# Kernel optimization log

Measured on AMD Instinct MI355X. Metric: run time of the kernel, lower is better.

## Reference

```python
import jax, jax.numpy as jnp
import numpy as np

MAXHD, MAXV, MINA, MAXA, DT = 100.0, 40.0, -4.0, 3.0, 0.1
NVEH, NT, H = 16384, 256, 20


def setup_inputs() -> dict:
    key = jax.random.key(0)
    ks = jax.random.split(key, 6)
    lead_speed = 10.0 + 5.0 * jax.random.normal(ks[0], (NVEH, NT), dtype=jnp.float32)
    lead_pos = 50.0 + 20.0 * jax.random.normal(ks[1], (NVEH, NT), dtype=jnp.float32)
    lead_inputs = jnp.stack([lead_pos, lead_speed], axis=2)  # (nveh, nt, 2)
    init_state = jnp.stack([
        5.0 * jax.random.normal(ks[2], (NVEH,), dtype=jnp.float32),
        10.0 + 2.0 * jax.random.normal(ks[3], (NVEH,), dtype=jnp.float32),
    ], axis=1)  # (nveh, 2) -> (pos, speed)
    return {
        "lead_inputs": lead_inputs,
        "init_state": init_state,
        "h0": jnp.zeros((NVEH, H), jnp.float32),
        "c0": jnp.zeros((NVEH, H), jnp.float32),
        "W": 0.3 * jax.random.normal(ks[4], (3, 4 * H), dtype=jnp.float32),
        "U": 0.2 * jax.random.normal(ks[5], (H, 4 * H), dtype=jnp.float32),
        "b": jnp.concatenate([jnp.zeros(H), jnp.ones(H), jnp.zeros(2 * H)]).astype(jnp.float32),  # unit forget bias
        "Wd": 0.3 * jax.random.normal(jax.random.fold_in(key, 7), (H, 1), dtype=jnp.float32),
        "bd": jnp.zeros((1,), jnp.float32),
    }


def reference(lead_inputs, init_state, h0, c0, W, U, b, Wd, bd):
    def step(carry, lead):
        pos, speed, h, c = carry
        curhd = (lead[:, 0] - pos) / MAXHD
        lead_v = lead[:, 1] / MAXV
        norm_v = speed / MAXV
        x = jnp.stack([curhd, norm_v, lead_v], axis=1)  # (nveh, 3)
        z = x @ W + h @ U + b  # (nveh, 4H), keras gate order i, f, g, o
        i, f, g, o = jnp.split(z, 4, axis=1)
        c = jax.nn.sigmoid(f) * c + jax.nn.sigmoid(i) * jnp.tanh(g)
        h = jax.nn.sigmoid(o) * jnp.tanh(c)
        out = (h @ Wd + bd)[:, 0]  # (nveh,)
        acc = (MAXA - MINA) * out + MINA
        speed = speed + DT * acc
        pos = pos + DT * acc  # faithful to source (uses acc, not speed)
        return (pos, speed, h, c), pos

    pos0, speed0 = init_state[:, 0], init_state[:, 1]
    (pos, speed, h, c), ys = jax.lax.scan(
        step, (pos0, speed0, h0, c0), jnp.swapaxes(lead_inputs, 0, 1))
    # tf.concat of nt (nveh,) tensors along -1 -> flat (nt*nveh,) in time-major order
    outputs = ys.reshape(-1)
    return outputs, speed, (h, c)
```

## Files before the change

### kernel.cpp

```cpp
#include <hip/hip_runtime.h>


#define NVEH 16384
#define NT   256
#define H    20

typedef float f32x4  __attribute__((ext_vector_type(4)));
typedef short bf16x8 __attribute__((ext_vector_type(8)));

#if __has_builtin(__builtin_amdgcn_exp2f)
#define EXP2(x) __builtin_amdgcn_exp2f(x)
#else
#define EXP2(x) __expf((x) * 0.69314718056f)
#endif
#define RCP(x) __builtin_amdgcn_rcpf(x)

__device__ __forceinline__ short f2bf(float f) {
    unsigned u = __builtin_bit_cast(unsigned, f);
    u += 0x7fffu + ((u >> 16) & 1u);
    return (short)(u >> 16);
}
__device__ __forceinline__ float bf2f(short s) {
    return __builtin_bit_cast(float, ((unsigned)(unsigned short)s) << 16);
}

__global__ __launch_bounds__(256, 1) void rnncf_kernel(
    const float* __restrict__ lead,
    const float* __restrict__ inits,
    const float* __restrict__ h0,
    const float* __restrict__ c0,
    const float* __restrict__ W,
    const float* __restrict__ U,
    const float* __restrict__ b,
    const float* __restrict__ Wd,
    const float* __restrict__ bd,
    float* __restrict__ out)
{
    __shared__ __attribute__((aligned(16))) short UT[96 * 32];

    const int tid  = threadIdx.x;
    const int lane = tid & 63;
    const int q    = lane >> 4;
    const int c    = lane & 15;
    const float L2E = 1.44269504f;
    const float N2L = -2.f * L2E;
    const float P2L =  2.f * L2E;
    const float IN2L = -0.34657359028f;
    const float bdv = bd[0];
    const float biasK = 7.f * bdv - 4.f;

    for (int idx = tid; idx < 96 * 32; idx += 256) {
        int row = idx >> 5, k = idx & 31;
        int T = row >> 4, m = row & 15;
        int kq = k >> 3, ko = k & 7;
        float v = 0.f;
        if (T < 5) {
            int g = m & 3, j = 5 * (m >> 2) + T;
            int col = g * 20 + j;
            if      (ko < 5)             v = U[(5 * kq + ko) * 80 + col];
            else if (ko == 6 && kq < 3)  v = W[kq * 80 + col];
            else if (ko == 6)            v = b[col];
            v *= (g == 2) ? (2.f * L2E) : L2E;
        } else if ((m & 3) == 0) {
            if      (ko < 5)  v = 7.f * Wd[5 * kq + ko];
            else if (ko == 5) v = 1.f;
        }
        UT[idx] = f2bf(v);
    }

    const int veh = blockIdx.x * 64 + (tid >> 6) * 16 + c;

    float wcn[5][4], wd7[5], w7b[5];
#pragma unroll
    for (int T = 0; T < 5; ++T) {
        int j = 5 * q + T;
#pragma unroll
        for (int g = 0; g < 4; ++g) {
            int col = g * 20 + j;
            wcn[T][g] = -(-0.001f * W[col] + 0.0025f * W[80 + col])
                      * ((g == 2) ? (2.f * L2E) : L2E);
        }
        float w7 = 7.f * Wd[j];
        wd7[T] = w7;
        w7b[T] = bf2f(f2bf(w7));
    }

    bf16x8 Bf = {0, 0, 0, 0, 0, 0, 0, 0};
    float cst2[5], hl[5];
    float rpart = 0.f, apart = 0.f;
#pragma unroll
    for (int T = 0; T < 5; ++T) {
        int j = 5 * q + T;
        float hv = h0[veh * H + j];
        cst2[T] = N2L * c0[veh * H + j];
        hl[T] = hv;
        short hb = f2bf(hv);
        float hi = bf2f(hb);
        Bf[T] = hb;
        rpart = __builtin_fmaf(hv, wd7[T], rpart);
        rpart = __builtin_fmaf(-hi, w7b[T], rpart);
        apart = __builtin_fmaf(hv, wd7[T], apart);
    }
    Bf[5] = f2bf(rpart);
    apart += __shfl_xor(apart, 16);
    apart += __shfl_xor(apart, 32);

    float pos = inits[veh * 2 + 0];
    float spd = inits[veh * 2 + 1];
    {
        float a = apart + biasK;
        pos -= 0.1f * a;
        spd -= 0.1f * a;
    }

    const float2* lp0 = (const float2*)lead + (long)veh * NT;
    {
        float2 lu = lp0[0];
        float xv = (q == 0) ? (lu.x - pos) * 0.01f
                 : (q == 1) ? spd * 0.025f
                            : lu.y * 0.025f;
        if (q < 3) Bf[6] = f2bf(xv);
        else       Bf[6] = (short)0x3F80;
    }
    float2 lA = lp0[1];
    float2 lB = lp0[2];

    __syncthreads();

    bf16x8 A[6];
#pragma unroll
    for (int T = 0; T < 6; ++T)
        A[T] = *(const bf16x8*)&UT[(T * 16 + c) * 32 + q * 8];

    for (int t = 0; t < NT; ++t) {
        float2 lu = lA;
        lA = lB;
        int tn = t + 3; tn = (tn < NT) ? tn : NT - 1;
        lB = lp0[tn];

        f32x4 zero = {0.f, 0.f, 0.f, 0.f};
        f32x4 z5 = __builtin_amdgcn_mfma_f32_16x16x32_bf16(A[5], Bf, zero, 0, 0, 0);
        f32x4 z[5];
#pragma unroll
        for (int T = 0; T < 5; ++T)
            z[T] = __builtin_amdgcn_mfma_f32_16x16x32_bf16(A[T], Bf, zero, 0, 0, 0);

        float acc = z5[0] + biasK;
        pos = __builtin_fmaf(0.1f, acc, pos);
        spd = __builtin_fmaf(0.1f, acc, spd);
        if (q == 1 && t > 0)
            out[(size_t)(t - 1) * NVEH + veh] = pos;

        {
            float xv = (q == 0) ? (lu.x - pos) * 0.01f
                     : (q == 1) ? spd * 0.025f
                                : lu.y * 0.025f;
            if (q < 3) Bf[6] = f2bf(xv);
        }

        float rq = 0.f;
#pragma unroll
        for (int T = 0; T < 5; ++T) {
            float ei = EXP2(__builtin_fmaf(acc, wcn[T][0], -z[T][0]));
            float ef = EXP2(__builtin_fmaf(acc, wcn[T][1], -z[T][1]));
            float eg = EXP2(__builtin_fmaf(acc, wcn[T][2], -z[T][2]));
            float eo = EXP2(__builtin_fmaf(acc, wcn[T][3], -z[T][3]));
            float ff  = RCP(1.f + ef);
            float Rig = RCP((1.f + ei) * (1.f + eg));
            float uu  = __builtin_fmaf(P2L, eg, N2L);
            float c2  = __builtin_fmaf(ff, cst2[T], uu * Rig);
            cst2[T] = c2;
            float ec = EXP2(__builtin_fminf(c2, 80.f));
            float Roc = RCP((1.f + eo) * (1.f + ec));
            float hh = (1.f - ec) * Roc;
            hl[T] = hh;
            unsigned u = __builtin_bit_cast(unsigned, hh);
            unsigned r = u + 0x7fffu + ((u >> 16) & 1u);
            Bf[T] = (short)(r >> 16);
            float hi = __builtin_bit_cast(float, r & 0xffff0000u);
            rq = __builtin_fmaf(hh, wd7[T], rq);
            rq = __builtin_fmaf(-hi, w7b[T], rq);
        }
        Bf[5] = f2bf(rq);
    }

    float ap = 0.f;
#pragma unroll
    for (int T = 0; T < 5; ++T) ap = __builtin_fmaf(hl[T], wd7[T], ap);
    ap += __shfl_xor(ap, 16);
    ap += __shfl_xor(ap, 32);
    float accF = ap + biasK;
    if (q == 1) out[(size_t)(NT - 1) * NVEH + veh] = pos + 0.1f * accF;
    if (q == 2) out[(size_t)NT * NVEH + veh]       = spd + 0.1f * accF;

    const int oH = NT * NVEH + NVEH;
    const int oC = oH + NVEH * H;
#pragma unroll
    for (int T = 0; T < 5; ++T) {
        int j = 5 * q + T;
        out[oH + veh * H + j] = hl[T];
        out[oC + veh * H + j] = cst2[T] * IN2L;
    }
}

extern "C" void kernel_launch(void* const* d_in, const int* in_sizes, int n_in,
                              void* d_out, int out_size, void* d_ws, size_t ws_size,
                              hipStream_t stream) {
    const float* lead  = (const float*)d_in[0];
    const float* inits = (const float*)d_in[1];
    const float* h0    = (const float*)d_in[2];
    const float* c0    = (const float*)d_in[3];
    const float* W     = (const float*)d_in[4];
    const float* U     = (const float*)d_in[5];
    const float* b     = (const float*)d_in[6];
    const float* Wd    = (const float*)d_in[7];
    const float* bd    = (const float*)d_in[8];
    float* out = (float*)d_out;

    rnncf_kernel<<<NVEH / 64, 256, 0, stream>>>(lead, inits, h0, c0, W, U, b, Wd, bd, out);
}
```

Measured before the change: 210.0 us.

## Replace MFMA-folded dense output with in-loop shuffle reduction and simpler gate math

Removes the sixth MFMA tile that folded the dense output projection and its bf16 residual correction into the recurrent matmul. The acceleration correction terms (wcn) that compensated for the one-step lag are dropped. Acceleration is now computed exactly each step with a per-lane dot product and two cross-lane shuffles. The gate update is also restructured to use a single combined reciprocal for the forget/input/cell gates. This puts the shuffle reduction back on the serial critical path of every step, in exchange for one fewer MFMA and fewer FMAs and reciprocals.

```diff
diff --git a/kernel.cpp b/kernel.cpp
--- a/kernel.cpp
+++ b/kernel.cpp
@@ -20,9 +20,6 @@
     u += 0x7fffu + ((u >> 16) & 1u);
     return (short)(u >> 16);
 }
-__device__ __forceinline__ float bf2f(short s) {
-    return __builtin_bit_cast(float, ((unsigned)(unsigned short)s) << 16);
-}
 
 __global__ __launch_bounds__(256, 1) void rnncf_kernel(
     const float* __restrict__ lead,
@@ -36,7 +33,7 @@
     const float* __restrict__ bd,
     float* __restrict__ out)
 {
-    __shared__ __attribute__((aligned(16))) short UT[96 * 32];
+    __shared__ __attribute__((aligned(16))) short UT[80 * 32];
 
     const int tid  = threadIdx.x;
     const int lane = tid & 63;
@@ -46,72 +43,41 @@
     const float N2L = -2.f * L2E;
     const float P2L =  2.f * L2E;
     const float IN2L = -0.34657359028f;
-    const float bdv = bd[0];
-    const float biasK = 7.f * bdv - 4.f;
+    const float biasK = 7.f * bd[0] - 4.f;
 
-    for (int idx = tid; idx < 96 * 32; idx += 256) {
+    for (int idx = tid; idx < 80 * 32; idx += 256) {
         int row = idx >> 5, k = idx & 31;
         int T = row >> 4, m = row & 15;
         int kq = k >> 3, ko = k & 7;
+        int g = m & 3, j = 5 * (m >> 2) + T;
+        int col = g * 20 + j;
         float v = 0.f;
-        if (T < 5) {
-            int g = m & 3, j = 5 * (m >> 2) + T;
-            int col = g * 20 + j;
-            if      (ko < 5)             v = U[(5 * kq + ko) * 80 + col];
-            else if (ko == 6 && kq < 3)  v = W[kq * 80 + col];
-            else if (ko == 6)            v = b[col];
-            v *= (g == 2) ? (2.f * L2E) : L2E;
-        } else if ((m & 3) == 0) {
-            if      (ko < 5)  v = 7.f * Wd[5 * kq + ko];
-            else if (ko == 5) v = 1.f;
-        }
+        if      (ko < 5)             v = U[(5 * kq + ko) * 80 + col];
+        else if (ko == 6 && kq < 3)  v = W[kq * 80 + col];
+        else if (ko == 6)            v = b[col];
+        v *= (g == 2) ? (2.f * L2E) : L2E;
         UT[idx] = f2bf(v);
     }
 
     const int veh = blockIdx.x * 64 + (tid >> 6) * 16 + c;
 
-    float wcn[5][4], wd7[5], w7b[5];
+    float wd7[5];
 #pragma unroll
-    for (int T = 0; T < 5; ++T) {
-        int j = 5 * q + T;
-#pragma unroll
-        for (int g = 0; g < 4; ++g) {
-            int col = g * 20 + j;
-            wcn[T][g] = -(-0.001f * W[col] + 0.0025f * W[80 + col])
-                      * ((g == 2) ? (2.f * L2E) : L2E);
-        }
-        float w7 = 7.f * Wd[j];
-        wd7[T] = w7;
-        w7b[T] = bf2f(f2bf(w7));
-    }
+    for (int T = 0; T < 5; ++T) wd7[T] = 7.f * Wd[5 * q + T];
 
     bf16x8 Bf = {0, 0, 0, 0, 0, 0, 0, 0};
     float cst2[5], hl[5];
-    float rpart = 0.f, apart = 0.f;
 #pragma unroll
     for (int T = 0; T < 5; ++T) {
         int j = 5 * q + T;
         float hv = h0[veh * H + j];
         cst2[T] = N2L * c0[veh * H + j];
         hl[T] = hv;
-        short hb = f2bf(hv);
-        float hi = bf2f(hb);
-        Bf[T] = hb;
-        rpart = __builtin_fmaf(hv, wd7[T], rpart);
-        rpart = __builtin_fmaf(-hi, w7b[T], rpart);
-        apart = __builtin_fmaf(hv, wd7[T], apart);
+        Bf[T] = f2bf(hv);
     }
-    Bf[5] = f2bf(rpart);
-    apart += __shfl_xor(apart, 16);
-    apart += __shfl_xor(apart, 32);
 
     float pos = inits[veh * 2 + 0];
     float spd = inits[veh * 2 + 1];
-    {
-        float a = apart + biasK;
-        pos -= 0.1f * a;
-        spd -= 0.1f * a;
-    }
 
     const float2* lp0 = (const float2*)lead + (long)veh * NT;
     {
@@ -127,9 +93,9 @@
 
     __syncthreads();
 
-    bf16x8 A[6];
+    bf16x8 A[5];
 #pragma unroll
-    for (int T = 0; T < 6; ++T)
+    for (int T = 0; T < 5; ++T)
         A[T] = *(const bf16x8*)&UT[(T * 16 + c) * 32 + q * 8];
 
     for (int t = 0; t < NT; ++t) {
@@ -139,59 +105,47 @@
         lB = lp0[tn];
 
         f32x4 zero = {0.f, 0.f, 0.f, 0.f};
-        f32x4 z5 = __builtin_amdgcn_mfma_f32_16x16x32_bf16(A[5], Bf, zero, 0, 0, 0);
         f32x4 z[5];
 #pragma unroll
         for (int T = 0; T < 5; ++T)
             z[T] = __builtin_amdgcn_mfma_f32_16x16x32_bf16(A[T], Bf, zero, 0, 0, 0);
 
-        float acc = z5[0] + biasK;
+#pragma unroll
+        for (int T = 0; T < 5; ++T) {
+            float ei = EXP2(-z[T][0]);
+            float ef = EXP2(-z[T][1]);
+            float eg = EXP2(-z[T][2]);
+            float eo = EXP2(-z[T][3]);
+            float pi = 1.f + ei, pf = 1.f + ef, pg = 1.f + eg, po = 1.f + eo;
+            float pig = pi * pg;
+            float R3  = RCP(pf * pig);
+            float uu  = __builtin_fmaf(P2L, eg, N2L);
+            float c2  = R3 * __builtin_fmaf(pig, cst2[T], uu * pf);
+            cst2[T] = c2;
+            float ec  = EXP2(__builtin_fminf(c2, 80.f));
+            float Roc = RCP(po * (1.f + ec));
+            float hh  = (1.f - ec) * Roc;
+            hl[T] = hh;
+            Bf[T] = f2bf(hh);
+        }
+
+        float p0 = __builtin_fmaf(hl[1], wd7[1], hl[0] * wd7[0]);
+        float p1 = __builtin_fmaf(hl[3], wd7[3], hl[2] * wd7[2]);
+        float ap = __builtin_fmaf(hl[4], wd7[4], p0 + p1);
+        ap += __shfl_xor(ap, 16);
+        ap += __shfl_xor(ap, 32);
+        float acc = ap + biasK;
         pos = __builtin_fmaf(0.1f, acc, pos);
         spd = __builtin_fmaf(0.1f, acc, spd);
-        if (q == 1 && t > 0)
-            out[(size_t)(t - 1) * NVEH + veh] = pos;
+        if (q == 1) out[(size_t)t * NVEH + veh] = pos;
 
-        {
-            float xv = (q == 0) ? (lu.x - pos) * 0.01f
-                     : (q == 1) ? spd * 0.025f
-                                : lu.y * 0.025f;
-            if (q < 3) Bf[6] = f2bf(xv);
-        }
-
-        float rq = 0.f;
-#pragma unroll
-        for (int T = 0; T < 5; ++T) {
-            float ei = EXP2(__builtin_fmaf(acc, wcn[T][0], -z[T][0]));
-            float ef = EXP2(__builtin_fmaf(acc, wcn[T][1], -z[T][1]));
-            float eg = EXP2(__builtin_fmaf(acc, wcn[T][2], -z[T][2]));
-            float eo = EXP2(__builtin_fmaf(acc, wcn[T][3], -z[T][3]));
-            float ff  = RCP(1.f + ef);
-            float Rig = RCP((1.f + ei) * (1.f + eg));
-            float uu  = __builtin_fmaf(P2L, eg, N2L);
-            float c2  = __builtin_fmaf(ff, cst2[T], uu * Rig);
-            cst2[T] = c2;
-            float ec = EXP2(__builtin_fminf(c2, 80.f));
-            float Roc = RCP((1.f + eo) * (1.f + ec));
-            float hh = (1.f - ec) * Roc;
-            hl[T] = hh;
-            unsigned u = __builtin_bit_cast(unsigned, hh);
-            unsigned r = u + 0x7fffu + ((u >> 16) & 1u);
-            Bf[T] = (short)(r >> 16);
-            float hi = __builtin_bit_cast(float, r & 0xffff0000u);
-            rq = __builtin_fmaf(hh, wd7[T], rq);
-            rq = __builtin_fmaf(-hi, w7b[T], rq);
-        }
-        Bf[5] = f2bf(rq);
+        float xv = (q == 0) ? (lu.x - pos) * 0.01f
+                 : (q == 1) ? spd * 0.025f
+                            : lu.y * 0.025f;
+        if (q < 3) Bf[6] = f2bf(xv);
     }
 
-    float ap = 0.f;
-#pragma unroll
-    for (int T = 0; T < 5; ++T) ap = __builtin_fmaf(hl[T], wd7[T], ap);
-    ap += __shfl_xor(ap, 16);
-    ap += __shfl_xor(ap, 32);
-    float accF = ap + biasK;
-    if (q == 1) out[(size_t)(NT - 1) * NVEH + veh] = pos + 0.1f * accF;
-    if (q == 2) out[(size_t)NT * NVEH + veh]       = spd + 0.1f * accF;
+    if (q == 2) out[(size_t)NT * NVEH + veh] = spd;
 
     const int oH = NT * NVEH + NVEH;
     const int oC = oH + NVEH * H;
```

After: 227.7 us. +8.4%, slower.
